# Kernel tuning notes

Measured on AMD Instinct MI355X. Metric: run time of the kernel, lower is better.

Reference implementation:

```python
import jax, jax.numpy as jnp
import numpy as np

J = 8          # number of octaves
Q = 8          # wavelets per octave (first order)
T = 16384      # signal length (power of two)
B = 4          # batch size
XI_MAX = 0.35  # center frequency of the mother wavelet (cycles/sample)


def _filters():
    """Frequency-domain Morlet-like analytic filterbank + Gaussian lowpass."""
    om = np.arange(T) / T                                   # normalized freqs in [0,1)
    # first-order: J*Q log-spaced analytic bandpass filters
    k1 = np.arange(J * Q)
    xi1 = XI_MAX * 2.0 ** (-k1 / Q)                         # (N1,) center freqs
    sig1 = xi1 * (2.0 ** (1.0 / Q) - 1.0)                   # ~1/Q-octave bandwidth
    psi1 = np.exp(-((om[None, :] - xi1[:, None]) ** 2) / (2.0 * sig1[:, None] ** 2))
    # second-order: J octave-spaced (Q2=1) wider filters
    k2 = np.arange(J).astype(np.float64)
    xi2 = XI_MAX * 2.0 ** (-k2)                             # (N2,)
    sig2 = xi2 * 0.5                                        # octave bandwidth
    psi2 = np.exp(-((om[None, :] - xi2[:, None]) ** 2) / (2.0 * sig2[:, None] ** 2))
    # lowpass phi at scale 2^J (symmetric on the circle)
    d = np.minimum(om, 1.0 - om)
    sig_phi = XI_MAX * 2.0 ** (-J)
    phi = np.exp(-(d ** 2) / (2.0 * sig_phi ** 2))
    # valid second-order paths: xi2 < xi1 (equivalent of j2 > j1)
    mask = (xi2[None, :] < xi1[:, None])                    # (N1, N2) bool
    return (jnp.asarray(psi1, jnp.float32), jnp.asarray(psi2, jnp.float32),
            jnp.asarray(phi, jnp.float32), jnp.asarray(mask))


def setup_inputs() -> dict:
    key = jax.random.key(0)
    x = jax.random.normal(key, (B, 1, T), dtype=jnp.float32)
    psi1_hat, psi2_hat, phi_hat, mask = _filters()
    return {"x": x, "psi1_hat": psi1_hat, "psi2_hat": psi2_hat,
            "phi_hat": phi_hat, "mask": mask, "stride": 2 ** J}


def reference(x, psi1_hat, psi2_hat, phi_hat, mask, stride):
    # x: (B,1,T); psi1_hat: (N1,T); psi2_hat: (N2,T); phi_hat: (T,); mask: (N1,N2)
    X = jnp.fft.fft(x)                                       # (B,1,T) complex
    lp = lambda h: jnp.real(jnp.fft.ifft(h * phi_hat))[..., ::stride]  # lowpass + subsample
    # zeroth order
    S0 = lp(X)[:, :, None, :]                                # (B,1,1,T')
    # first order: bandpass -> modulus
    U1 = jnp.abs(jnp.fft.ifft(X[:, :, None, :] * psi1_hat))  # (B,1,N1,T)
    U1h = jnp.fft.fft(U1)
    S1 = lp(U1h)                                             # (B,1,N1,T')
    # second order: bandpass the first-order envelopes -> modulus
    U2 = jnp.abs(jnp.fft.ifft(U1h[:, :, :, None, :] * psi2_hat))  # (B,1,N1,N2,T)
    S2 = lp(jnp.fft.fft(U2)) * mask[None, None, :, :, None]  # (B,1,N1,N2,T')
    b, c, n1, n2, tp = S2.shape
    S2 = S2.reshape(b, c, n1 * n2, tp)
    Sx = jnp.concatenate([S0, S1, S2], axis=2)               # (B,C=1,P,T')
    # torch module: (B,C,T,F) -> (B,1,T,F*C); with C=1 this is the identity reshape
    return Sx.reshape(b, 1, Sx.shape[2], Sx.shape[3] * c)
```

## Files before the change

### kernel.cpp

```cpp
#include <hip/hip_runtime.h>
#include <math.h>

#define T_LEN   16384
#define NTH     512
#define TPRIME  64
#define NPATH   577
#define INV_T   (1.0f/16384.0f)
#define TWO_PI  6.28318530717958647692f
#define NW      640
#define NH      (NW + 1)
#define C8C     0.92387953251128675613f
#define C8S     0.38268343236508977173f

__device__ __forceinline__ int rev4(int i) {
    int r = 0;
#pragma unroll
    for (int p = 0; p < 7; ++p) { r = (r << 2) | (i & 3); i >>= 2; }
    return r;
}
__device__ __forceinline__ int IDX(int i) {
    return i ^ ((i >> 4) & 15) ^ ((i >> 8) & 15);
}
#define S6 IDX
__device__ __forceinline__ int UIDX(int n) {
    return n ^ ((n >> 5) & 31) ^ ((n >> 10) & 31);
}
__device__ __forceinline__ int US(int n) { return n ^ ((n >> 5) & 31); }

__device__ __forceinline__ void inv_bf4(float2& A0, float2& A1, float2& A2, float2& A3,
                                        float c1, float s1) {
    float sr = A0.x + A1.x + A2.x + A3.x, si = A0.y + A1.y + A2.y + A3.y;
    float tr = A0.x - A1.y - A2.x + A3.y, ti = A0.y + A1.x - A2.y - A3.x;
    float ur = A0.x - A1.x + A2.x - A3.x, ui = A0.y - A1.y + A2.y - A3.y;
    float vr = A0.x + A1.y - A2.x - A3.y, vi = A0.y - A1.x - A2.y + A3.x;
    float c2 = c1*c1 - s1*s1, s2 = 2.f*c1*s1;
    float c3 = c1*c2 - s1*s2, s3 = c1*s2 + s1*c2;
    A0 = make_float2(sr, si);
    A1 = make_float2(tr*c1 - ti*s1, tr*s1 + ti*c1);
    A2 = make_float2(ur*c2 - ui*s2, ur*s2 + ui*c2);
    A3 = make_float2(vr*c3 - vi*s3, vr*s3 + vi*c3);
}
__device__ __forceinline__ void fwd_bf4(float2& B0, float2& B1, float2& B2, float2& B3,
                                        float c1, float s1) {
    float c2 = c1*c1 - s1*s1, s2 = 2.f*c1*s1;
    float c3 = c1*c2 - s1*s2, s3 = c1*s2 + s1*c2;
    float trr = B1.x*c1 + B1.y*s1, tii = B1.y*c1 - B1.x*s1;
    float urr = B2.x*c2 + B2.y*s2, uii = B2.y*c2 - B2.x*s2;
    float vrr = B3.x*c3 + B3.y*s3, vii = B3.y*c3 - B3.x*s3;
    float s0r = B0.x, s0i = B0.y;
    B0 = make_float2(s0r + trr + urr + vrr, s0i + tii + uii + vii);
    B1 = make_float2(s0r + tii - urr - vii, s0i - trr - uii + vrr);
    B2 = make_float2(s0r - trr + urr - vrr, s0i - tii + uii - vii);
    B3 = make_float2(s0r - tii - urr + vii, s0i + trr - uii - vrr);
}

template<int Q>
__device__ __forceinline__ void inv_group16(float2* v, int jp) {
    float a0 = (float)jp * (TWO_PI / (float)(4 * Q));
    float cw, sw; __sincosf(a0, &sw, &cw);
    float c = cw, s = sw;
#pragma unroll
    for (int rp = 0; rp < 4; ++rp) {
        inv_bf4(v[rp], v[4+rp], v[8+rp], v[12+rp], c, s);
        float cn = c*C8C - s*C8S, sn = c*C8S + s*C8C;
        c = cn; s = sn;
    }
    float b0 = (float)jp * (TWO_PI / (float)Q);
    float cb, sb; __sincosf(b0, &sb, &cb);
#pragma unroll
    for (int r = 0; r < 4; ++r)
        inv_bf4(v[4*r], v[4*r+1], v[4*r+2], v[4*r+3], cb, sb);
}
template<int QA>
__device__ __forceinline__ void fwd_group16(float2* v, int jp) {
    float aA = (float)jp * (TWO_PI / (float)(4 * QA));
    float cA, sA; __sincosf(aA, &sA, &cA);
#pragma unroll
    for (int r = 0; r < 4; ++r)
        fwd_bf4(v[4*r], v[4*r+1], v[4*r+2], v[4*r+3], cA, sA);
    float aB = (float)jp * (TWO_PI / (float)(16 * QA));
    float cB, sB; __sincosf(aB, &sB, &cB);
    float c = cB, s = sB;
#pragma unroll
    for (int rp = 0; rp < 4; ++rp) {
        fwd_bf4(v[rp], v[4+rp], v[8+rp], v[12+rp], c, s);
        float cn = c*C8C - s*C8S, sn = c*C8S + s*C8C;
        c = cn; s = sn;
    }
}

template<int LQ>
__device__ void inv_pass16(float2* buf) {
    const int q = 1 << LQ, qp = q >> 2;
    __syncthreads();
#pragma unroll
    for (int it = 0; it < 2; ++it) {
        int g2 = threadIdx.x + it * NTH;
        int jp = g2 & (qp - 1);
        int base = ((g2 >> (LQ - 2)) << (LQ + 2)) | jp;
        float2 v[16];
#pragma unroll
        for (int r = 0; r < 4; ++r)
#pragma unroll
            for (int rp = 0; rp < 4; ++rp)
                v[4*r+rp] = buf[IDX(base + r*q + rp*qp)];
        inv_group16<(1 << LQ)>(v, jp);
#pragma unroll
        for (int r = 0; r < 4; ++r)
#pragma unroll
            for (int rp = 0; rp < 4; ++rp)
                buf[IDX(base + r*q + rp*qp)] = v[4*r+rp];
    }
}

__device__ void inv_pass16_g(const float2* __restrict__ src, const float* __restrict__ filt,
                             float2* buf, int clo, int chi) {
#pragma unroll 1
    for (int it = 0; it < 2; ++it) {
        int jp = threadIdx.x + it * NTH;
        float2 v[16];
#pragma unroll
        for (int r = 0; r < 4; ++r)
#pragma unroll
            for (int rp = 0; rp < 4; ++rp) {
                int ch = 4*r + rp;
                if (ch >= clo && ch <= chi) {
                    int i = jp + r*4096 + rp*1024;
                    float2 a = src[i]; float p = filt[i];
                    v[4*r+rp] = make_float2(a.x*p, a.y*p);
                } else {
                    v[4*r+rp] = make_float2(0.f, 0.f);
                }
            }
        inv_group16<4096>(v, jp);
#pragma unroll
        for (int r = 0; r < 4; ++r)
#pragma unroll
            for (int rp = 0; rp < 4; ++rp)
                buf[IDX(jp + r*4096 + rp*1024)] = v[4*r+rp];
        asm volatile("" ::: "memory");
    }
}

__device__ void mod_fwd4(float2* buf) {
    __syncthreads();
#pragma unroll
    for (int it = 0; it < 8; ++it) {
        int base = (threadIdx.x + it * NTH) << 2;
        float2 a0 = buf[IDX(base)], a1 = buf[IDX(base+1)], a2 = buf[IDX(base+2)], a3 = buf[IDX(base+3)];
        inv_bf4(a0, a1, a2, a3, 1.0f, 0.0f);
        float2 b0 = make_float2(sqrtf(a0.x*a0.x + a0.y*a0.y) * INV_T, 0.f);
        float2 b1 = make_float2(sqrtf(a1.x*a1.x + a1.y*a1.y) * INV_T, 0.f);
        float2 b2 = make_float2(sqrtf(a2.x*a2.x + a2.y*a2.y) * INV_T, 0.f);
        float2 b3 = make_float2(sqrtf(a3.x*a3.x + a3.y*a3.y) * INV_T, 0.f);
        fwd_bf4(b0, b1, b2, b3, 1.0f, 0.0f);
        buf[IDX(base)] = b0; buf[IDX(base+1)] = b1; buf[IDX(base+2)] = b2; buf[IDX(base+3)] = b3;
    }
}

template<int LQA>
__device__ void fwd_pass16(float2* buf) {
    const int qA = 1 << LQA, qB = 4 * qA;
    __syncthreads();
#pragma unroll
    for (int it = 0; it < 2; ++it) {
        int g2 = threadIdx.x + it * NTH;
        int jp = g2 & (qA - 1);
        int base = ((g2 >> LQA) << (LQA + 4)) | jp;
        float2 v[16];
#pragma unroll
        for (int r = 0; r < 4; ++r)
#pragma unroll
            for (int rp = 0; rp < 4; ++rp)
                v[4*r+rp] = buf[IDX(base + r*qB + rp*qA)];
        fwd_group16<(1 << LQA)>(v, jp);
#pragma unroll
        for (int r = 0; r < 4; ++r)
#pragma unroll
            for (int rp = 0; rp < 4; ++rp)
                buf[IDX(base + r*qB + rp*qA)] = v[4*r+rp];
    }
}

__device__ void fwd_last_store_zs(float2* buf, float2* __restrict__ gout, int nchunks,
                                  float2* zs) {
    __syncthreads();
#pragma unroll 1
    for (int it = 0; it < 2; ++it) {
        int jp = threadIdx.x + it * NTH;
        float2 v[16];
#pragma unroll
        for (int r = 0; r < 4; ++r)
#pragma unroll
            for (int rp = 0; rp < 4; ++rp)
                v[4*r+rp] = buf[IDX(jp + r*4096 + rp*1024)];
        fwd_group16<1024>(v, jp);
        if (it == 0 && jp < 124) zs[jp] = v[0];
#pragma unroll
        for (int r = 0; r < 4; ++r)
#pragma unroll
            for (int rp = 0; rp < 4; ++rp) {
                int ch = 4*r + rp;
                if (ch < nchunks)
                    gout[jp + r*4096 + rp*1024] = v[4*r+rp];
            }
        asm volatile("" ::: "memory");
    }
}

__global__ __launch_bounds__(512) void k1_prep(const float* __restrict__ x,
                                               const float* __restrict__ phi,
                                               float2* __restrict__ Z,
                                               float* __restrict__ hws,
                                               int B2) {
    const int bi = blockIdx.x;
    if (bi < B2) {
        const int b = bi >> 1;
        const int jp = ((bi & 1) << 9) | threadIdx.x;
        const float* xb = x + (size_t)b * T_LEN;
        float2* Zb = Z + (size_t)b * T_LEN;
        float2 v[16];
#pragma unroll
        for (int r = 0; r < 4; ++r)
#pragma unroll
            for (int rp = 0; rp < 4; ++rp)
                v[4*r+rp] = make_float2(xb[jp + r*4096 + rp*1024], 0.f);
        inv_group16<4096>(v, jp);
#pragma unroll
        for (int r = 0; r < 4; ++r)
#pragma unroll
            for (int rp = 0; rp < 4; ++rp)
                Zb[jp + r*4096 + rp*1024] = v[4*r+rp];
    } else {
        const int d = (bi - B2) * 8 + (threadIdx.x >> 6);
        const int l = threadIdx.x & 63;
        float p = 0.f;
#pragma unroll
        for (int j = 0; j < 8; ++j) {
            int w = l + 64 * j;
            int k = (w < 256) ? w : (15872 + w);
            int r = (k * d) & (T_LEN - 1);
            p += phi[k] * __cosf((float)r * (TWO_PI / (float)T_LEN));
        }
        p += __shfl_xor(p, 1);  p += __shfl_xor(p, 2);  p += __shfl_xor(p, 4);
        p += __shfl_xor(p, 8);  p += __shfl_xor(p, 16); p += __shfl_xor(p, 32);
        if (l == 0 && d <= NW) hws[d] = p * INV_T;
    }
}

__global__ __launch_bounds__(256) void k2_chunk_s0(const float2* __restrict__ Z,
                                                   const float* __restrict__ x,
                                                   const float* __restrict__ hws,
                                                   float2* __restrict__ wsX,
                                                   float* __restrict__ out,
                                                   int B4) {
    __shared__ float2 lds[4096];
    __shared__ float hl[NH];
    const int bi = blockIdx.x;
    if (bi < B4) {
        const int b = bi >> 2;
        const int c0 = (bi & 3) << 12;
        const float2* Zb = Z + (size_t)b * T_LEN + c0;
        for (int i = threadIdx.x; i < 4096; i += 256) lds[IDX(i)] = Zb[i];
        {
            __syncthreads();
            int g = threadIdx.x;
            int jp = g & 63, base = ((g >> 6) << 10) | jp;
            float2 v[16];
#pragma unroll
            for (int r = 0; r < 4; ++r)
#pragma unroll
                for (int rp = 0; rp < 4; ++rp)
                    v[4*r+rp] = lds[IDX(base + r*256 + rp*64)];
            inv_group16<256>(v, jp);
#pragma unroll
            for (int r = 0; r < 4; ++r)
#pragma unroll
                for (int rp = 0; rp < 4; ++rp)
                    lds[IDX(base + r*256 + rp*64)] = v[4*r+rp];
        }
        {
            __syncthreads();
            int g = threadIdx.x;
            int jp = g & 3, base = ((g >> 2) << 6) | jp;
            float2 v[16];
#pragma unroll
            for (int r = 0; r < 4; ++r)
#pragma unroll
                for (int rp = 0; rp < 4; ++rp)
                    v[4*r+rp] = lds[IDX(base + r*16 + rp*4)];
            inv_group16<16>(v, jp);
#pragma unroll
            for (int r = 0; r < 4; ++r)
#pragma unroll
                for (int rp = 0; rp < 4; ++rp)
                    lds[IDX(base + r*16 + rp*4)] = v[4*r+rp];
        }
        __syncthreads();
        float2* W = wsX + (size_t)b * T_LEN;
#pragma unroll
        for (int it = 0; it < 4; ++it) {
            int bl = (threadIdx.x + it * 256) << 2;
            float2 a0 = lds[IDX(bl)], a1 = lds[IDX(bl+1)], a2 = lds[IDX(bl+2)], a3 = lds[IDX(bl+3)];
            inv_bf4(a0, a1, a2, a3, 1.0f, 0.0f);
            int rb = rev4(c0 + bl);
            W[rb]         = make_float2(a0.x, -a0.y);
            W[rb + 4096]  = make_float2(a1.x, -a1.y);
            W[rb + 8192]  = make_float2(a2.x, -a2.y);
            W[rb + 12288] = make_float2(a3.x, -a3.y);
        }
    } else {
        const int q = bi - B4;
        const int b = q >> 3;
        const int m0 = (q & 7) << 3;
        for (int i = threadIdx.x; i < NH; i += 256) hl[i] = hws[i];
        __syncthreads();
        const float* xb = x + (size_t)b * T_LEN;
        const int m = m0 + (threadIdx.x >> 5);
        const int s = threadIdx.x & 31;
        const int c = m << 8;
        float acc = 0.f;
        for (int e = -NW + s; e <= NW; e += 32) {
            int n = (c + e) & (T_LEN - 1);
            int a = e < 0 ? -e : e;
            acc += hl[a] * xb[n];
        }
        acc += __shfl_xor(acc, 1);  acc += __shfl_xor(acc, 2);
        acc += __shfl_xor(acc, 4);  acc += __shfl_xor(acc, 8);
        acc += __shfl_xor(acc, 16);
        if (s == 0) out[(size_t)b * (NPATH * TPRIME) + m] = acc;
    }
}

__global__ __launch_bounds__(NTH)
__attribute__((amdgpu_waves_per_eu(1, 2)))
void pass_b(const float2* __restrict__ wsX,
            const float* __restrict__ psi1,
            const float* __restrict__ phi,
            float2* __restrict__ wsU,
            float* __restrict__ out) {
    __shared__ float2 buf[T_LEN];
    __shared__ float2 zs[128];
    const int blk = blockIdx.x;
    const int b = blk >> 6, n1 = blk & 63;
    float xi1T = 5734.4f * exp2f(-(float)n1 / 8.0f);
    int clo = (int)(0.40f * xi1T) >> 10;
    int chi = ((int)(1.60f * xi1T)) >> 10; if (chi > 15) chi = 15;
    inv_pass16_g(wsX + (size_t)b * T_LEN, psi1 + (size_t)n1 * T_LEN, buf, clo, chi);
    inv_pass16<8>(buf);
    inv_pass16<4>(buf);
    mod_fwd4(buf);
    fwd_pass16<2>(buf);
    fwd_pass16<6>(buf);
    const int n2min = (n1 >> 3) + 1;
    int nch = 0;
    if (n2min <= 7) {
        int S = 24084 >> n2min;
        nch = (S >> 10) + 1; if (nch > 10) nch = 10;
    }
    fwd_last_store_zs(buf, wsU + (size_t)blk * T_LEN, nch, zs);
    __syncthreads();
    const int m = threadIdx.x >> 3;
    const int s = threadIdx.x & 7;
    float acc = 0.f;
    for (int k = 1 + s; k < 124; k += 8) {
        float ph = phi[k];
        float2 z = zs[k];
        float ang = (float)((k * m) & 63) * (TWO_PI / 64.0f);
        float sn, cs; __sincosf(ang, &sn, &cs);
        acc += 2.0f * ph * (z.x * cs - z.y * sn);
    }
    acc += __shfl_xor(acc, 1);
    acc += __shfl_xor(acc, 2);
    acc += __shfl_xor(acc, 4);
    if (s == 0) {
        acc += zs[0].x * phi[0];
        out[(size_t)b * (NPATH * TPRIME) + (size_t)(1 + n1) * TPRIME + m] = acc * INV_T;
    }
}

__global__ __launch_bounds__(512) void k4_med2(const float2* __restrict__ wsU,
                                               const float* __restrict__ psi2,
                                               const float* __restrict__ hws,
                                               float* __restrict__ out) {
    __shared__ float2 sc2[8192];
    __shared__ float h2s[321];
    const int tj = threadIdx.x;
    const int hh = tj >> 8, t = tj & 255;
    const int idx = blockIdx.x % 24, b = blockIdx.x / 24;
    const int n2 = (idx < 8) ? 1 : 2;
    const int n1 = (idx < 8) ? idx : idx - 8;
    for (int i = tj; i < 321; i += 512) h2s[i] = 2.0f * hws[2 * i];
    float2* sc = sc2 + (hh << 12);
    const float2* Ub = wsU + (size_t)((b << 6) | n1) * T_LEN;
    const float* p2 = psi2 + (size_t)n2 * T_LEN;
    const int lim = (n2 == 1) ? 10240 : 6144;
    float2 v[16];
#pragma unroll
    for (int r = 0; r < 4; ++r) {
#pragma unroll
        for (int rp = 0; rp < 4; ++rp) {
            int i = t + r*1024 + rp*256;
            float2 y0 = Ub[i]; float q0 = p2[i];
            float ar = y0.x * q0, ai = y0.y * q0;
            if (i + 4096 < lim) {
                float2 y1 = Ub[i + 4096]; float q1 = p2[i + 4096];
                if (hh == 0) { ar += y1.x*q1; ai += y1.y*q1; }
                else         { ar -= y1.x*q1; ai -= y1.y*q1; }
            }
            if (i + 8192 < lim) {
                float2 y2 = Ub[i + 8192]; float q2 = p2[i + 8192];
                ar += y2.x*q2; ai += y2.y*q2;
            }
            if (hh == 1) {
                float ang = (float)i * (TWO_PI / 8192.0f);
                float sn, cs; __sincosf(ang, &sn, &cs);
                float nr = ar*cs - ai*sn, ni = ar*sn + ai*cs;
                ar = nr; ai = ni;
            }
            v[4*r+rp] = make_float2(ar, ai);
        }
        asm volatile("" ::: "memory");
    }
    inv_group16<1024>(v, t);
#pragma unroll
    for (int r = 0; r < 4; ++r)
#pragma unroll
        for (int rp = 0; rp < 4; ++rp)
            sc[S6(t + r*1024 + rp*256)] = v[4*r+rp];
    __syncthreads();
    {
        int jp = t & 15, base = ((t >> 4) << 8) | jp;
#pragma unroll
        for (int r = 0; r < 4; ++r)
#pragma unroll
            for (int rp = 0; rp < 4; ++rp)
                v[4*r+rp] = sc[S6(base + r*64 + rp*16)];
        inv_group16<64>(v, jp);
#pragma unroll
        for (int r = 0; r < 4; ++r)
#pragma unroll
            for (int rp = 0; rp < 4; ++rp)
                sc[S6(base + r*64 + rp*16)] = v[4*r+rp];
    }
    __syncthreads();
    float mg[16];
    {
        int base = t << 4;
#pragma unroll
        for (int r = 0; r < 4; ++r)
#pragma unroll
            for (int rp = 0; rp < 4; ++rp)
                v[4*r+rp] = sc[S6(base + 4*r + rp)];
        inv_group16<4>(v, 0);
#pragma unroll
        for (int k = 0; k < 16; ++k)
            mg[k] = sqrtf(v[k].x*v[k].x + v[k].y*v[k].y) * INV_T;
    }
    __syncthreads();
    float* u8s = (float*)sc2;
    int rt = ((t & 3) << 6) | (((t >> 2) & 3) << 4) | (((t >> 4) & 3) << 2) | (t >> 6);
#pragma unroll
    for (int r = 0; r < 4; ++r)
#pragma unroll
        for (int rp = 0; rp < 4; ++rp) {
            int pos = rp*1024 + r*256 + rt;
            u8s[UIDX(2 * pos + hh)] = mg[4*r+rp];
        }
    __syncthreads();
    const int m = tj >> 3, s = tj & 7;
    float acc = 0.f;
    for (int e = -320 + s; e <= 320; e += 8) {
        int n = (128*m + e) & 8191;
        int a = e < 0 ? -e : e;
        acc += h2s[a] * u8s[UIDX(n)];
    }
    acc += __shfl_xor(acc, 1);
    acc += __shfl_xor(acc, 2);
    acc += __shfl_xor(acc, 4);
    if (s == 0)
        out[(size_t)b * (NPATH * TPRIME) + (size_t)(65 + (n1 << 3) + n2) * TPRIME + m] = acc;
}

__global__ __launch_bounds__(256) void k4_small(const float2* __restrict__ wsU,
                                                const float* __restrict__ psi2,
                                                const float* __restrict__ hws,
                                                float* __restrict__ out) {
    __shared__ float2 buf[4096];
    __shared__ float hd[161];
    const int t = threadIdx.x;
    const int idx = blockIdx.x % 488, b = blockIdx.x / 488;

    if (idx >= 200) {
        int z = idx - 200;
        int g = 0, cum = 0;
#pragma unroll
        for (int gg = 0; gg < 8; ++gg) {
            int c = 8 * (gg + 1);
            if (z >= cum + c) { cum += c; g = gg + 1; }
        }
        int zz = z - cum;
        int n1 = g * 8 + zz / (g + 1);
        int n2 = zz % (g + 1);
        if (t < TPRIME)
            out[(size_t)b * (NPATH * TPRIME) + (size_t)(65 + (n1 << 3) + n2) * TPRIME + t] = 0.f;
        return;
    }

    const int p = idx;
    int n1, n2;
    if      (p < 24)  { n2 = 3; n1 = p; }
    else if (p < 56)  { n2 = 4; n1 = p - 24; }
    else if (p < 96)  { n2 = 5; n1 = p - 56; }
    else if (p < 144) { n2 = 6; n1 = p - 96; }
    else              { n2 = 7; n1 = p - 144; }
    if (t < 161) hd[t] = 4.0f * hws[4 * t];
    const int kc = ((((int)(24084.0f * exp2f(-(float)n2))) >> 10) + 1) << 2;
    const float2* Ub = wsU + (size_t)((b << 6) | n1) * T_LEN;
    const float* p2 = psi2 + (size_t)n2 * T_LEN;
    float2 v[16];
#pragma unroll
    for (int r = 0; r < 4; ++r)
#pragma unroll
        for (int rp = 0; rp < 4; ++rp) {
            int ch = 4*r + rp;
            if (ch < kc) {
                int i = t + r*1024 + rp*256;
                float2 u = Ub[i]; float pp = p2[i];
                v[4*r+rp] = make_float2(u.x*pp, u.y*pp);
            } else {
                v[4*r+rp] = make_float2(0.f, 0.f);
            }
        }
    inv_group16<1024>(v, t);
#pragma unroll
    for (int r = 0; r < 4; ++r)
#pragma unroll
        for (int rp = 0; rp < 4; ++rp)
            buf[S6(t + r*1024 + rp*256)] = v[4*r+rp];
    __syncthreads();
    {
        int jp = t & 15, base = ((t >> 4) << 8) | jp;
#pragma unroll
        for (int r = 0; r < 4; ++r)
#pragma unroll
            for (int rp = 0; rp < 4; ++rp)
                v[4*r+rp] = buf[S6(base + r*64 + rp*16)];
        inv_group16<64>(v, jp);
#pragma unroll
        for (int r = 0; r < 4; ++r)
#pragma unroll
            for (int rp = 0; rp < 4; ++rp)
                buf[S6(base + r*64 + rp*16)] = v[4*r+rp];
    }
    __syncthreads();
    float mg[16];
    {
        int base = t << 4;
#pragma unroll
        for (int r = 0; r < 4; ++r)
#pragma unroll
            for (int rp = 0; rp < 4; ++rp)
                v[4*r+rp] = buf[S6(base + 4*r + rp)];
        inv_group16<4>(v, 0);
#pragma unroll
        for (int k = 0; k < 16; ++k)
            mg[k] = sqrtf(v[k].x*v[k].x + v[k].y*v[k].y) * INV_T;
    }
    __syncthreads();
    float* uf = (float*)buf;
    int rt = ((t & 3) << 6) | (((t >> 2) & 3) << 4) | (((t >> 4) & 3) << 2) | (t >> 6);
#pragma unroll
    for (int r = 0; r < 4; ++r)
#pragma unroll
        for (int rp = 0; rp < 4; ++rp)
            uf[US(rp*1024 + r*256 + rt)] = mg[4*r+rp];
    __syncthreads();
    const int m = t >> 2, s = t & 3;
    float acc = 0.f;
    for (int e = -160 + s; e <= 160; e += 4) {
        int n = (64*m + e) & 4095;
        int a = e < 0 ? -e : e;
        acc += hd[a] * uf[US(n)];
    }
    acc += __shfl_xor(acc, 1);
    acc += __shfl_xor(acc, 2);
    if (s == 0)
        out[(size_t)b * (NPATH * TPRIME) + (size_t)(65 + (n1 << 3) + n2) * TPRIME + m] = acc;
}

extern "C" void kernel_launch(void* const* d_in, const int* in_sizes, int n_in,
                              void* d_out, int out_size, void* d_ws, size_t ws_size,
                              hipStream_t stream) {
    const float* x    = (const float*)d_in[0];
    const float* psi1 = (const float*)d_in[1];
    const float* psi2 = (const float*)d_in[2];
    const float* phi  = (const float*)d_in[3];
    float* out = (float*)d_out;

    const int B = in_sizes[0] / T_LEN;

    float*  hws = (float*)d_ws;
    float2* wsX = (float2*)((char*)d_ws + 4096);
    float2* wsU = (float2*)((char*)d_ws + 4096 + (size_t)B * T_LEN * sizeof(float2));
    float2* Z   = wsU;

    k1_prep<<<2 * B + 81, 512, 0, stream>>>(x, phi, Z, hws, 2 * B);
    k2_chunk_s0<<<4 * B + 8 * B, 256, 0, stream>>>(Z, x, hws, wsX, out, 4 * B);
    pass_b<<<B * 64, NTH, 0, stream>>>(wsX, psi1, phi, wsU, out);
    k4_med2<<<B * 24, 512, 0, stream>>>(wsU, psi2, hws, out);
    k4_small<<<B * 488, 256, 0, stream>>>(wsU, psi2, hws, out);
}
```

Before: 91.49 us.

## Split fused first-order FFT pass into three kernels for more parallelism

Result: slower. 114.9 us (+25.6%).

```diff
diff --git a/kernel.cpp b/kernel.cpp
--- a/kernel.cpp
+++ b/kernel.cpp
@@ -86,125 +86,6 @@
         fwd_bf4(v[rp], v[4+rp], v[8+rp], v[12+rp], c, s);
         float cn = c*C8C - s*C8S, sn = c*C8S + s*C8C;
         c = cn; s = sn;
-    }
-}
-
-template<int LQ>
-__device__ void inv_pass16(float2* buf) {
-    const int q = 1 << LQ, qp = q >> 2;
-    __syncthreads();
-#pragma unroll
-    for (int it = 0; it < 2; ++it) {
-        int g2 = threadIdx.x + it * NTH;
-        int jp = g2 & (qp - 1);
-        int base = ((g2 >> (LQ - 2)) << (LQ + 2)) | jp;
-        float2 v[16];
-#pragma unroll
-        for (int r = 0; r < 4; ++r)
-#pragma unroll
-            for (int rp = 0; rp < 4; ++rp)
-                v[4*r+rp] = buf[IDX(base + r*q + rp*qp)];
-        inv_group16<(1 << LQ)>(v, jp);
-#pragma unroll
-        for (int r = 0; r < 4; ++r)
-#pragma unroll
-            for (int rp = 0; rp < 4; ++rp)
-                buf[IDX(base + r*q + rp*qp)] = v[4*r+rp];
-    }
-}
-
-__device__ void inv_pass16_g(const float2* __restrict__ src, const float* __restrict__ filt,
-                             float2* buf, int clo, int chi) {
-#pragma unroll 1
-    for (int it = 0; it < 2; ++it) {
-        int jp = threadIdx.x + it * NTH;
-        float2 v[16];
-#pragma unroll
-        for (int r = 0; r < 4; ++r)
-#pragma unroll
-            for (int rp = 0; rp < 4; ++rp) {
-                int ch = 4*r + rp;
-                if (ch >= clo && ch <= chi) {
-                    int i = jp + r*4096 + rp*1024;
-                    float2 a = src[i]; float p = filt[i];
-                    v[4*r+rp] = make_float2(a.x*p, a.y*p);
-                } else {
-                    v[4*r+rp] = make_float2(0.f, 0.f);
-                }
-            }
-        inv_group16<4096>(v, jp);
-#pragma unroll
-        for (int r = 0; r < 4; ++r)
-#pragma unroll
-            for (int rp = 0; rp < 4; ++rp)
-                buf[IDX(jp + r*4096 + rp*1024)] = v[4*r+rp];
-        asm volatile("" ::: "memory");
-    }
-}
-
-__device__ void mod_fwd4(float2* buf) {
-    __syncthreads();
-#pragma unroll
-    for (int it = 0; it < 8; ++it) {
-        int base = (threadIdx.x + it * NTH) << 2;
-        float2 a0 = buf[IDX(base)], a1 = buf[IDX(base+1)], a2 = buf[IDX(base+2)], a3 = buf[IDX(base+3)];
-        inv_bf4(a0, a1, a2, a3, 1.0f, 0.0f);
-        float2 b0 = make_float2(sqrtf(a0.x*a0.x + a0.y*a0.y) * INV_T, 0.f);
-        float2 b1 = make_float2(sqrtf(a1.x*a1.x + a1.y*a1.y) * INV_T, 0.f);
-        float2 b2 = make_float2(sqrtf(a2.x*a2.x + a2.y*a2.y) * INV_T, 0.f);
-        float2 b3 = make_float2(sqrtf(a3.x*a3.x + a3.y*a3.y) * INV_T, 0.f);
-        fwd_bf4(b0, b1, b2, b3, 1.0f, 0.0f);
-        buf[IDX(base)] = b0; buf[IDX(base+1)] = b1; buf[IDX(base+2)] = b2; buf[IDX(base+3)] = b3;
-    }
-}
-
-template<int LQA>
-__device__ void fwd_pass16(float2* buf) {
-    const int qA = 1 << LQA, qB = 4 * qA;
-    __syncthreads();
-#pragma unroll
-    for (int it = 0; it < 2; ++it) {
-        int g2 = threadIdx.x + it * NTH;
-        int jp = g2 & (qA - 1);
-        int base = ((g2 >> LQA) << (LQA + 4)) | jp;
-        float2 v[16];
-#pragma unroll
-        for (int r = 0; r < 4; ++r)
-#pragma unroll
-            for (int rp = 0; rp < 4; ++rp)
-                v[4*r+rp] = buf[IDX(base + r*qB + rp*qA)];
-        fwd_group16<(1 << LQA)>(v, jp);
-#pragma unroll
-        for (int r = 0; r < 4; ++r)
-#pragma unroll
-            for (int rp = 0; rp < 4; ++rp)
-                buf[IDX(base + r*qB + rp*qA)] = v[4*r+rp];
-    }
-}
-
-__device__ void fwd_last_store_zs(float2* buf, float2* __restrict__ gout, int nchunks,
-                                  float2* zs) {
-    __syncthreads();
-#pragma unroll 1
-    for (int it = 0; it < 2; ++it) {
-        int jp = threadIdx.x + it * NTH;
-        float2 v[16];
-#pragma unroll
-        for (int r = 0; r < 4; ++r)
-#pragma unroll
-            for (int rp = 0; rp < 4; ++rp)
-                v[4*r+rp] = buf[IDX(jp + r*4096 + rp*1024)];
-        fwd_group16<1024>(v, jp);
-        if (it == 0 && jp < 124) zs[jp] = v[0];
-#pragma unroll
-        for (int r = 0; r < 4; ++r)
-#pragma unroll
-            for (int rp = 0; rp < 4; ++rp) {
-                int ch = 4*r + rp;
-                if (ch < nchunks)
-                    gout[jp + r*4096 + rp*1024] = v[4*r+rp];
-            }
-        asm volatile("" ::: "memory");
     }
 }
 
@@ -332,36 +213,163 @@
     }
 }
 
-__global__ __launch_bounds__(NTH)
-__attribute__((amdgpu_waves_per_eu(1, 2)))
-void pass_b(const float2* __restrict__ wsX,
-            const float* __restrict__ psi1,
-            const float* __restrict__ phi,
-            float2* __restrict__ wsU,
-            float* __restrict__ out) {
-    __shared__ float2 buf[T_LEN];
-    __shared__ float2 zs[128];
-    const int blk = blockIdx.x;
-    const int b = blk >> 6, n1 = blk & 63;
+__global__ __launch_bounds__(512) void kb1(const float2* __restrict__ wsX,
+                                           const float* __restrict__ psi1,
+                                           float2* __restrict__ wsU) {
+    const int path = blockIdx.x >> 1, half = blockIdx.x & 1;
+    const int b = path >> 6, n1 = path & 63;
+    const int jp = (half << 9) | threadIdx.x;
     float xi1T = 5734.4f * exp2f(-(float)n1 / 8.0f);
     int clo = (int)(0.40f * xi1T) >> 10;
     int chi = ((int)(1.60f * xi1T)) >> 10; if (chi > 15) chi = 15;
-    inv_pass16_g(wsX + (size_t)b * T_LEN, psi1 + (size_t)n1 * T_LEN, buf, clo, chi);
-    inv_pass16<8>(buf);
-    inv_pass16<4>(buf);
-    mod_fwd4(buf);
-    fwd_pass16<2>(buf);
-    fwd_pass16<6>(buf);
+    const float2* Xb = wsX + (size_t)b * T_LEN;
+    const float* ps = psi1 + (size_t)n1 * T_LEN;
+    float2 v[16];
+#pragma unroll
+    for (int r = 0; r < 4; ++r)
+#pragma unroll
+        for (int rp = 0; rp < 4; ++rp) {
+            int ch = 4*r + rp;
+            if (ch >= clo && ch <= chi) {
+                int i = jp + r*4096 + rp*1024;
+                float2 a = Xb[i]; float p = ps[i];
+                v[4*r+rp] = make_float2(a.x*p, a.y*p);
+            } else {
+                v[4*r+rp] = make_float2(0.f, 0.f);
+            }
+        }
+    inv_group16<4096>(v, jp);
+    float2* Zr = wsU + (size_t)path * T_LEN;
+#pragma unroll
+    for (int r = 0; r < 4; ++r)
+#pragma unroll
+        for (int rp = 0; rp < 4; ++rp)
+            Zr[jp + r*4096 + rp*1024] = v[4*r+rp];
+}
+
+__global__ __launch_bounds__(256) void kb2(float2* __restrict__ wsU) {
+    __shared__ float2 lds[4096];
+    const int path = blockIdx.x >> 2, c0 = (blockIdx.x & 3) << 12;
+    const int t = threadIdx.x;
+    float2* Zr = wsU + (size_t)path * T_LEN + c0;
+    for (int i = t; i < 4096; i += 256) lds[IDX(i)] = Zr[i];
+    {
+        __syncthreads();
+        int jp = t & 63, base = ((t >> 6) << 10) | jp;
+        float2 v[16];
+#pragma unroll
+        for (int r = 0; r < 4; ++r)
+#pragma unroll
+            for (int rp = 0; rp < 4; ++rp)
+                v[4*r+rp] = lds[IDX(base + r*256 + rp*64)];
+        inv_group16<256>(v, jp);
+#pragma unroll
+        for (int r = 0; r < 4; ++r)
+#pragma unroll
+            for (int rp = 0; rp < 4; ++rp)
+                lds[IDX(base + r*256 + rp*64)] = v[4*r+rp];
+    }
+    {
+        __syncthreads();
+        int jp = t & 3, base = ((t >> 2) << 6) | jp;
+        float2 v[16];
+#pragma unroll
+        for (int r = 0; r < 4; ++r)
+#pragma unroll
+            for (int rp = 0; rp < 4; ++rp)
+                v[4*r+rp] = lds[IDX(base + r*16 + rp*4)];
+        inv_group16<16>(v, jp);
+#pragma unroll
+        for (int r = 0; r < 4; ++r)
+#pragma unroll
+            for (int rp = 0; rp < 4; ++rp)
+                lds[IDX(base + r*16 + rp*4)] = v[4*r+rp];
+    }
+    __syncthreads();
+#pragma unroll
+    for (int it = 0; it < 4; ++it) {
+        int bl = (t + it * 256) << 2;
+        float2 a0 = lds[IDX(bl)], a1 = lds[IDX(bl+1)], a2 = lds[IDX(bl+2)], a3 = lds[IDX(bl+3)];
+        inv_bf4(a0, a1, a2, a3, 1.0f, 0.0f);
+        float2 b0 = make_float2(sqrtf(a0.x*a0.x + a0.y*a0.y) * INV_T, 0.f);
+        float2 b1 = make_float2(sqrtf(a1.x*a1.x + a1.y*a1.y) * INV_T, 0.f);
+        float2 b2 = make_float2(sqrtf(a2.x*a2.x + a2.y*a2.y) * INV_T, 0.f);
+        float2 b3 = make_float2(sqrtf(a3.x*a3.x + a3.y*a3.y) * INV_T, 0.f);
+        fwd_bf4(b0, b1, b2, b3, 1.0f, 0.0f);
+        lds[IDX(bl)] = b0; lds[IDX(bl+1)] = b1; lds[IDX(bl+2)] = b2; lds[IDX(bl+3)] = b3;
+    }
+    {
+        __syncthreads();
+        int jp = t & 3, base = ((t >> 2) << 6) | jp;
+        float2 v[16];
+#pragma unroll
+        for (int r = 0; r < 4; ++r)
+#pragma unroll
+            for (int rp = 0; rp < 4; ++rp)
+                v[4*r+rp] = lds[IDX(base + r*16 + rp*4)];
+        fwd_group16<4>(v, jp);
+#pragma unroll
+        for (int r = 0; r < 4; ++r)
+#pragma unroll
+            for (int rp = 0; rp < 4; ++rp)
+                lds[IDX(base + r*16 + rp*4)] = v[4*r+rp];
+    }
+    {
+        __syncthreads();
+        int jp = t & 63, base = ((t >> 6) << 10) | jp;
+        float2 v[16];
+#pragma unroll
+        for (int r = 0; r < 4; ++r)
+#pragma unroll
+            for (int rp = 0; rp < 4; ++rp)
+                v[4*r+rp] = lds[IDX(base + r*256 + rp*64)];
+        fwd_group16<64>(v, jp);
+#pragma unroll
+        for (int r = 0; r < 4; ++r)
+#pragma unroll
+            for (int rp = 0; rp < 4; ++rp)
+                lds[IDX(base + r*256 + rp*64)] = v[4*r+rp];
+    }
+    __syncthreads();
+    for (int i = t; i < 4096; i += 256) Zr[i] = lds[IDX(i)];
+}
+
+__global__ __launch_bounds__(512) void kb3(float2* __restrict__ wsU,
+                                           const float* __restrict__ phi,
+                                           float* __restrict__ out) {
+    __shared__ float2 zs[128];
+    const int path = blockIdx.x >> 1, half = blockIdx.x & 1;
+    const int b = path >> 6, n1 = path & 63;
+    const int t = threadIdx.x;
     const int n2min = (n1 >> 3) + 1;
     int nch = 0;
     if (n2min <= 7) {
         int S = 24084 >> n2min;
         nch = (S >> 10) + 1; if (nch > 10) nch = 10;
     }
-    fwd_last_store_zs(buf, wsU + (size_t)blk * T_LEN, nch, zs);
-    __syncthreads();
-    const int m = threadIdx.x >> 3;
-    const int s = threadIdx.x & 7;
+    if (half == 1 && nch == 0) return;
+    const int jp = (half << 9) | t;
+    float2* Zr = wsU + (size_t)path * T_LEN;
+    float2 v[16];
+#pragma unroll
+    for (int r = 0; r < 4; ++r)
+#pragma unroll
+        for (int rp = 0; rp < 4; ++rp)
+            v[4*r+rp] = Zr[jp + r*4096 + rp*1024];
+    fwd_group16<1024>(v, jp);
+    if (half == 0 && jp < 124) zs[jp] = v[0];
+#pragma unroll
+    for (int r = 0; r < 4; ++r)
+#pragma unroll
+        for (int rp = 0; rp < 4; ++rp) {
+            int ch = 4*r + rp;
+            if (ch < nch)
+                Zr[jp + r*4096 + rp*1024] = v[4*r+rp];
+        }
+    if (half != 0) return;
+    __syncthreads();
+    const int m = t >> 3;
+    const int s = t & 7;
     float acc = 0.f;
     for (int k = 1 + s; k < 124; k += 8) {
         float ph = phi[k];
@@ -607,7 +615,9 @@
 
     k1_prep<<<2 * B + 81, 512, 0, stream>>>(x, phi, Z, hws, 2 * B);
     k2_chunk_s0<<<4 * B + 8 * B, 256, 0, stream>>>(Z, x, hws, wsX, out, 4 * B);
-    pass_b<<<B * 64, NTH, 0, stream>>>(wsX, psi1, phi, wsU, out);
+    kb1<<<B * 128, 512, 0, stream>>>(wsX, psi1, wsU);
+    kb2<<<B * 256, 256, 0, stream>>>(wsU);
+    kb3<<<B * 128, 512, 0, stream>>>(wsU, phi, out);
     k4_med2<<<B * 24, 512, 0, stream>>>(wsU, psi2, hws, out);
     k4_small<<<B * 488, 256, 0, stream>>>(wsU, psi2, hws, out);
 }
```

## Remap middle FFT passes to wave-private chunks and drop block barriers

Applied to the files above, without the earlier changes.

Measured after the change: 91.09 us. About the same (-0.4%).

```diff
diff --git a/kernel.cpp b/kernel.cpp
--- a/kernel.cpp
+++ b/kernel.cpp
@@ -113,6 +113,30 @@
     }
 }
 
+template<int LQ>
+__device__ void inv_pass16_nb(float2* buf) {
+    const int q = 1 << LQ, qp = q >> 2;
+#pragma unroll
+    for (int it = 0; it < 2; ++it) {
+        int g2 = threadIdx.x + it * NTH;
+        int jp = g2 & (qp - 1);
+        int base = ((g2 >> (LQ - 2)) << (LQ + 2)) | jp;
+        float2 v[16];
+#pragma unroll
+        for (int r = 0; r < 4; ++r)
+#pragma unroll
+            for (int rp = 0; rp < 4; ++rp)
+                v[4*r+rp] = buf[IDX(base + r*q + rp*qp)];
+        inv_group16<(1 << LQ)>(v, jp);
+#pragma unroll
+        for (int r = 0; r < 4; ++r)
+#pragma unroll
+            for (int rp = 0; rp < 4; ++rp)
+                buf[IDX(base + r*q + rp*qp)] = v[4*r+rp];
+    }
+    asm volatile("" ::: "memory");
+}
+
 __device__ void inv_pass16_g(const float2* __restrict__ src, const float* __restrict__ filt,
                              float2* buf, int clo, int chi) {
 #pragma unroll 1
@@ -142,26 +166,29 @@
     }
 }
 
-__device__ void mod_fwd4(float2* buf) {
-    __syncthreads();
-#pragma unroll
-    for (int it = 0; it < 8; ++it) {
-        int base = (threadIdx.x + it * NTH) << 2;
-        float2 a0 = buf[IDX(base)], a1 = buf[IDX(base+1)], a2 = buf[IDX(base+2)], a3 = buf[IDX(base+3)];
-        inv_bf4(a0, a1, a2, a3, 1.0f, 0.0f);
-        float2 b0 = make_float2(sqrtf(a0.x*a0.x + a0.y*a0.y) * INV_T, 0.f);
-        float2 b1 = make_float2(sqrtf(a1.x*a1.x + a1.y*a1.y) * INV_T, 0.f);
-        float2 b2 = make_float2(sqrtf(a2.x*a2.x + a2.y*a2.y) * INV_T, 0.f);
-        float2 b3 = make_float2(sqrtf(a3.x*a3.x + a3.y*a3.y) * INV_T, 0.f);
-        fwd_bf4(b0, b1, b2, b3, 1.0f, 0.0f);
-        buf[IDX(base)] = b0; buf[IDX(base+1)] = b1; buf[IDX(base+2)] = b2; buf[IDX(base+3)] = b3;
-    }
+__device__ void mod_fwd4_wp(float2* buf) {
+#pragma unroll
+    for (int it = 0; it < 2; ++it) {
+        int g = (threadIdx.x >> 2) + it * 128;
+#pragma unroll
+        for (int k = 0; k < 4; ++k) {
+            int base = g * 64 + ((threadIdx.x & 3) + k * 4) * 4;
+            float2 a0 = buf[IDX(base)], a1 = buf[IDX(base+1)], a2 = buf[IDX(base+2)], a3 = buf[IDX(base+3)];
+            inv_bf4(a0, a1, a2, a3, 1.0f, 0.0f);
+            float2 b0 = make_float2(sqrtf(a0.x*a0.x + a0.y*a0.y) * INV_T, 0.f);
+            float2 b1 = make_float2(sqrtf(a1.x*a1.x + a1.y*a1.y) * INV_T, 0.f);
+            float2 b2 = make_float2(sqrtf(a2.x*a2.x + a2.y*a2.y) * INV_T, 0.f);
+            float2 b3 = make_float2(sqrtf(a3.x*a3.x + a3.y*a3.y) * INV_T, 0.f);
+            fwd_bf4(b0, b1, b2, b3, 1.0f, 0.0f);
+            buf[IDX(base)] = b0; buf[IDX(base+1)] = b1; buf[IDX(base+2)] = b2; buf[IDX(base+3)] = b3;
+        }
+    }
+    asm volatile("" ::: "memory");
 }
 
 template<int LQA>
-__device__ void fwd_pass16(float2* buf) {
+__device__ void fwd_pass16_nb(float2* buf) {
     const int qA = 1 << LQA, qB = 4 * qA;
-    __syncthreads();
 #pragma unroll
     for (int it = 0; it < 2; ++it) {
         int g2 = threadIdx.x + it * NTH;
@@ -180,6 +207,7 @@
             for (int rp = 0; rp < 4; ++rp)
                 buf[IDX(base + r*qB + rp*qA)] = v[4*r+rp];
     }
+    asm volatile("" ::: "memory");
 }
 
 __device__ void fwd_last_store_zs(float2* buf, float2* __restrict__ gout, int nchunks,
@@ -347,11 +375,12 @@
     int clo = (int)(0.40f * xi1T) >> 10;
     int chi = ((int)(1.60f * xi1T)) >> 10; if (chi > 15) chi = 15;
     inv_pass16_g(wsX + (size_t)b * T_LEN, psi1 + (size_t)n1 * T_LEN, buf, clo, chi);
-    inv_pass16<8>(buf);
-    inv_pass16<4>(buf);
-    mod_fwd4(buf);
-    fwd_pass16<2>(buf);
-    fwd_pass16<6>(buf);
+    __syncthreads();
+    inv_pass16_nb<8>(buf);
+    inv_pass16_nb<4>(buf);
+    mod_fwd4_wp(buf);
+    fwd_pass16_nb<2>(buf);
+    fwd_pass16_nb<6>(buf);
     const int n2min = (n1 >> 3) + 1;
     int nch = 0;
     if (n2min <= 7) {
```
